# Optimization experiments

Hardware: AMD Instinct MI355X
Metric: run time of the kernel (lower is better)

Reference implementation:

```python
import jax, jax.numpy as jnp
import numpy as np
from jax import lax

TWN_THRESHOLD_FACTOR = 0.05
BN_EPS = 1e-5


@jax.custom_vjp
def _ternary_quant(w, t):
    return (w > t).astype(w.dtype) - (w < -t).astype(w.dtype)

def _tq_fwd(w, t):
    mask = (w > t) | (w < -t)
    return _ternary_quant(w, t), mask

def _tq_bwd(mask, g):
    return (g * mask.astype(g.dtype), jnp.zeros((), g.dtype))

_ternary_quant.defvjp(_tq_fwd, _tq_bwd)


def quantize(w):
    # threshold is detached in the original (weight.detach().abs().max())
    t = TWN_THRESHOLD_FACTOR * jnp.max(jnp.abs(lax.stop_gradient(w)))
    return _ternary_quant(w, t)


def conv2d(x, w, b):
    # x: [N,C,H,W], w: [O,I,K,K], valid conv, stride 1
    y = lax.conv_general_dilated(x, w, (1, 1), 'VALID',
                                 dimension_numbers=('NCHW', 'OIHW', 'NCHW'))
    return y + b[None, :, None, None]


def maxpool2(x):
    return lax.reduce_window(x, -jnp.inf, lax.max,
                             (1, 1, 2, 2), (1, 1, 2, 2), 'VALID')


def bn2d(x, g, b):
    # training-mode batch norm over (N,H,W), biased variance
    m = jnp.mean(x, (0, 2, 3), keepdims=True)
    v = jnp.mean(jnp.square(x - m), (0, 2, 3), keepdims=True)
    return (x - m) * lax.rsqrt(v + BN_EPS) * g[None, :, None, None] + b[None, :, None, None]


def bn1d(x, g, b):
    m = jnp.mean(x, 0, keepdims=True)
    v = jnp.mean(jnp.square(x - m), 0, keepdims=True)
    return (x - m) * lax.rsqrt(v + BN_EPS) * g[None, :] + b[None, :]


def setup_inputs() -> dict:
    key = jax.random.key(0)
    ks = jax.random.split(key, 12)
    N = 4096
    inp = {
        'x': jax.random.normal(ks[0], (N, 1, 28, 28), jnp.float32),
        'w1': jax.random.normal(ks[1], (32, 1, 5, 5), jnp.float32) * 0.2,
        'b1': jnp.zeros((32,), jnp.float32),
        'g1': jnp.ones((32,), jnp.float32),
        'be1': jnp.zeros((32,), jnp.float32),
        'w2': jax.random.normal(ks[2], (64, 32, 5, 5), jnp.float32) * 0.05,
        'b2': jnp.zeros((64,), jnp.float32),
        'g2': jnp.ones((64,), jnp.float32),
        'be2': jnp.zeros((64,), jnp.float32),
        'wf1': jax.random.normal(ks[3], (512, 1024), jnp.float32) * 0.03,
        'bf1': jnp.zeros((512,), jnp.float32),
        'g3': jnp.ones((512,), jnp.float32),
        'be3': jnp.zeros((512,), jnp.float32),
        'wf2': jax.random.normal(ks[4], (10, 512), jnp.float32) * 0.04,
        'bf2': jnp.zeros((10,), jnp.float32),
    }
    return inp


def reference(x, w1, b1, g1, be1, w2, b2, g2, be2, wf1, bf1, g3, be3, wf2, bf2):
    h = jax.nn.relu(bn2d(conv2d(x, quantize(w1), b1), g1, be1))     # [N,32,24,24]
    h = maxpool2(h)                                                  # [N,32,12,12]
    h = jax.nn.relu(bn2d(conv2d(h, quantize(w2), b2), g2, be2))     # [N,64,8,8]
    h = maxpool2(h)                                                  # [N,64,4,4]
    h = h.reshape(h.shape[0], -1)                                    # [N,1024]
    h = jax.nn.relu(bn1d(h @ quantize(wf1).T + bf1, g3, be3))       # [N,512]
    return h @ quantize(wf2).T + bf2                                 # [N,10]
```

## Files before the change

kernel.cpp:

```cpp
#include <hip/hip_runtime.h>

#define TID ((int)threadIdx.x)
typedef unsigned short u16;
typedef short short8 __attribute__((ext_vector_type(8)));
typedef float f32x4 __attribute__((ext_vector_type(4)));

__device__ __forceinline__ u16 f2b(float f) {
    unsigned int x = __float_as_uint(f);
    return (u16)((x + 0x7fffu + ((x >> 16) & 1u)) >> 16);
}
__device__ __forceinline__ float b2f(u16 u) {
    return __uint_as_float(((unsigned int)u) << 16);
}
__device__ __forceinline__ unsigned int cvt_pk(float lo, float hi) {
    unsigned int r;
    asm("v_cvt_pk_bf16_f32 %0, %1, %2" : "=v"(r) : "v"(lo), "v"(hi));
    return r;
}
__device__ __forceinline__ float xmax32(float w) {
    unsigned int a = __float_as_uint(w), b = a;
    asm("v_permlane32_swap_b32 %0, %1" : "+v"(a), "+v"(b));
    return fmaxf(__uint_as_float(a), __uint_as_float(b));
}

static constexpr size_t OFF_QW1   = 0;
static constexpr size_t OFF_QWF2  = 3200;
static constexpr size_t OFF_TMAX  = 23680;
static constexpr size_t OFF_SUM1C = 23808;
static constexpr size_t OFF_SSQ1C = 24832;
static constexpr size_t OFF_SUM2  = 25856, OFF_SSQ2 = 26112;
static constexpr size_t OFF_SUM3  = 26368, OFF_SSQ3 = 28416;
static constexpr size_t STATS_BEG = 23680, STATS_END = 30464;
static constexpr size_t OFF_QW2C  = 30720;
static constexpr size_t OFF_QWF1C = 133120;
static constexpr size_t OFF_Y1P   = 1181696;
static constexpr size_t OFF_H2P   = 38930432;
static constexpr size_t OFF_Y3    = 47319040;

__global__ __launch_bounds__(256) void absmax_k(const float* w1, const float* w2,
                                                const float* wf1, const float* wf2,
                                                unsigned int* tmaxbits) {
    int bid = blockIdx.x;
    int b, lb, nb; const float* src; long n;
    if (bid < 1)        { b = 0; src = w1;  n = 800;    lb = bid;       nb = 1;   }
    else if (bid < 9)   { b = 1; src = w2;  n = 51200;  lb = bid - 1;   nb = 8;   }
    else if (bid < 265) { b = 2; src = wf1; n = 524288; lb = bid - 9;   nb = 256; }
    else                { b = 3; src = wf2; n = 5120;   lb = bid - 265; nb = 1;   }
    float m = 0.f;
    for (long i = (long)lb * 256 + TID; i < n; i += (long)nb * 256)
        m = fmaxf(m, fabsf(src[i]));
    __shared__ float red[256];
    red[TID] = m; __syncthreads();
    for (int s = 128; s > 0; s >>= 1) {
        if (TID < s) red[TID] = fmaxf(red[TID], red[TID + s]);
        __syncthreads();
    }
    if (TID == 0) atomicMax(&tmaxbits[b], __float_as_uint(red[0]));
}

__global__ __launch_bounds__(256) void quant_all_k(const float* w1, const float* w2,
                                                   const float* wf1, const float* wf2,
                                                   float* qw1, u16* qw2c, u16* qwf1c,
                                                   float* qwf2, const unsigned int* tmax) {
    int bid = blockIdx.x;
    if (bid < 4) {
        int i = bid * 256 + TID; if (i >= 800) return;
        float t = 0.05f * __uint_as_float(tmax[0]);
        float v = w1[i];
        qw1[i] = (v > t) ? 1.f : ((v < -t) ? -1.f : 0.f);
    } else if (bid < 204) {
        int i = (bid - 4) * 256 + TID;
        float t = 0.05f * __uint_as_float(tmax[1]);
        int ic = i & 31, oc = (i >> 5) & 63, sh = i >> 11;
        float v = w2[(oc * 32 + ic) * 25 + sh];
        qw2c[i] = (v > t) ? (u16)0x3F80 : ((v < -t) ? (u16)0xBF80 : (u16)0);
    } else if (bid < 2252) {
        int i = (bid - 204) * 256 + TID;
        float t = 0.05f * __uint_as_float(tmax[2]);
        float v = wf1[i];
        qwf1c[i] = (v > t) ? (u16)0x3F80 : ((v < -t) ? (u16)0xBF80 : (u16)0);
    } else {
        int i = (bid - 2252) * 256 + TID;
        float t = 0.05f * __uint_as_float(tmax[3]);
        float v = wf2[i];
        qwf2[i] = (v > t) ? 1.f : ((v < -t) ? -1.f : 0.f);
    }
}

__global__ __launch_bounds__(256) void conv1_fused_k(const float* __restrict__ x,
                                                     const float* __restrict__ qw1,
                                                     u16* __restrict__ y1p,
                                                     float* sum1c, float* ssq1c) {
    __shared__ __align__(16) u16 xs[16 * 1096];
    int gid = blockIdx.x;
    int sg = gid >> 2, ph = (gid >> 1) & 1, pch = gid & 1;
    int l = TID & 63, w = TID >> 6;
    int lm = l & 15, q = l >> 4;

    #pragma unroll
    for (int i = 0; i < 9; i++) {
        int idx = TID + i * 256;
        if (idx < 2192) reinterpret_cast<uint4*>(xs)[idx] = make_uint4(0, 0, 0, 0);
    }

    short8 B1[2], B2[2];
    #pragma unroll
    for (int c = 0; c < 2; c++) {
        union { short8 s; u16 h[8]; } b1, b2;
        int ch = c * 16 + lm;
        #pragma unroll
        for (int j = 0; j < 8; j++) {
            float v1 = 0.f, v2 = 0.f;
            if (j < 5) {
                v1 = qw1[ch * 25 + q * 5 + j];
                v2 = qw1[ch * 25 + 20 + j];
            }
            b1.h[j] = f2b(v1);
            b2.h[j] = (q == 0) ? f2b(v2) : (u16)0;
        }
        B1[c] = b1.s; B2[c] = b2.s;
    }
    __syncthreads();

    #pragma unroll
    for (int k = 0; k < 7; k++) {
        int i = TID + k * 256;
        int smp = i / 112, rem = i % 112;
        int row = rem / 7, c4 = (rem % 7) * 4;
        float4 v = *reinterpret_cast<const float4*>(
            x + (size_t)(sg * 16 + smp) * 784 + (12 * ph + row) * 28 + c4);
        unsigned int r0 = cvt_pk(v.x, v.y), r1 = cvt_pk(v.z, v.w);
        uint2 pk; pk.x = r0; pk.y = r1;
        *reinterpret_cast<uint2*>(xs + smp * 1096 + row * 32 + c4) = pk;
        u16 h[4] = {(u16)r0, (u16)(r0 >> 16), (u16)r1, (u16)(r1 >> 16)};
        u16* b1p = xs + smp * 1096 + 548 + row * 32;
        #pragma unroll
        for (int e = 0; e < 4; e++) {
            int c = c4 + e;
            if (c >= 1) b1p[c - 1] = h[e];
        }
    }
    __syncthreads();

    float s0 = 0.f, s1 = 0.f, q0 = 0.f, q1 = 0.f;
    int laneoff = lm * 1096;
    #pragma unroll 1
    for (int e = 0; e < 9; e++) {
        int pp = w * 9 + e;
        int prl = pp / 6, pcl = pp - prl * 6;
        f32x4 pm0 = {-3.0e38f, -3.0e38f, -3.0e38f, -3.0e38f};
        f32x4 pm1 = pm0;
        #pragma unroll
        for (int dyx = 0; dyx < 4; dyx++) {
            int dy = dyx >> 1, dx = dyx & 1;
            int oyl = 2 * prl + dy;
            int ox = 2 * (pch * 6 + pcl) + dx;
            int r = ox & 1, cb = ox - r;
            const u16* p1 = xs + laneoff + r * 548 + (oyl + q) * 32 + cb;
            const u16* p2 = xs + laneoff + r * 548 + (oyl + 4) * 32 + cb;
            union { short8 s; unsigned int u[4]; } a1, a2;
            #pragma unroll
            for (int t = 0; t < 4; t++) {
                a1.u[t] = *reinterpret_cast<const unsigned int*>(p1 + 2 * t);
                a2.u[t] = *reinterpret_cast<const unsigned int*>(p2 + 2 * t);
            }
            f32x4 d0 = {0.f, 0.f, 0.f, 0.f};
            d0 = __builtin_amdgcn_mfma_f32_16x16x32_bf16(a1.s, B1[0], d0, 0, 0, 0);
            d0 = __builtin_amdgcn_mfma_f32_16x16x32_bf16(a2.s, B2[0], d0, 0, 0, 0);
            f32x4 d1 = {0.f, 0.f, 0.f, 0.f};
            d1 = __builtin_amdgcn_mfma_f32_16x16x32_bf16(a1.s, B1[1], d1, 0, 0, 0);
            d1 = __builtin_amdgcn_mfma_f32_16x16x32_bf16(a2.s, B2[1], d1, 0, 0, 0);
            #pragma unroll
            for (int i = 0; i < 4; i++) {
                float v = d0[i]; s0 += v; q0 = fmaf(v, v, q0);
                float u = d1[i]; s1 += u; q1 = fmaf(u, u, q1);
            }
            pm0 = __builtin_elementwise_max(pm0, d0);
            pm1 = __builtin_elementwise_max(pm1, d1);
        }
        int ppg = (ph * 6 + prl) * 12 + (pch * 6 + pcl);
        #pragma unroll
        for (int i = 0; i < 4; i++) {
            size_t nb = (size_t)(sg * 16 + 4 * q + i) * 4608 + ppg * 32;
            unsigned int r = cvt_pk(pm0[i], pm1[i]);
            y1p[nb + lm]      = (u16)r;
            y1p[nb + 16 + lm] = (u16)(r >> 16);
        }
    }
    s0 += __shfl_xor(s0, 16); s0 += __shfl_xor(s0, 32);
    s1 += __shfl_xor(s1, 16); s1 += __shfl_xor(s1, 32);
    q0 += __shfl_xor(q0, 16); q0 += __shfl_xor(q0, 32);
    q1 += __shfl_xor(q1, 16); q1 += __shfl_xor(q1, 32);
    if (l < 16) {
        int slot = (blockIdx.x & 7) * 32;
        atomicAdd(&sum1c[slot + l], s0);
        atomicAdd(&sum1c[slot + 16 + l], s1);
        atomicAdd(&ssq1c[slot + l], q0);
        atomicAdd(&ssq1c[slot + 16 + l], q1);
    }
}

__global__ __launch_bounds__(256) void conv2_k(const u16* __restrict__ y1p,
                                               const u16* __restrict__ qw2c,
                                               u16* __restrict__ h2pre,
                                               const float* sum1c, const float* ssq1c,
                                               const float* g1, const float* be1,
                                               float* sum, float* ssq) {
    __shared__ float4 hsm4[1176];
    __shared__ float scs[32], shs[32];
    char* hsraw = (char*)hsm4;
    int n0 = blockIdx.x * 8;
    int l = TID & 63, wv = TID >> 6;
    int oc0 = wv * 16;
    int lm = l & 15, lr = (l >> 3) & 1, ox = l & 7, bq = l >> 4;
    if (TID < 32) {
        float s = 0.f, q = 0.f;
        #pragma unroll
        for (int r = 0; r < 8; r++) { s += sum1c[r * 32 + TID]; q += ssq1c[r * 32 + TID]; }
        float m = s * (1.f / 2359296.f);
        float v = q * (1.f / 2359296.f) - m * m;
        float sc = g1[TID] / sqrtf(v + 1e-5f);
        scs[TID] = sc; shs[TID] = be1[TID] - m * sc;
    }
    __syncthreads();
    float scR[8], shR[8];
    {
        int b = TID & 3;
        #pragma unroll
        for (int j = 0; j < 8; j++) { scR[j] = scs[b * 8 + j]; shR[j] = shs[b * 8 + j]; }
    }
    short8 bw[25];
    #pragma unroll
    for (int sh = 0; sh < 25; sh++)
        bw[sh] = *reinterpret_cast<const short8*>(qw2c + ((size_t)sh * 64 + oc0 + lm) * 32 + bq * 8);
    int xy[5];
    #pragma unroll
    for (int kx = 0; kx < 5; kx++) {
        int xx = ox + kx;
        xy[kx] = lr * 784 + xx * 64 + (((bq + (xx >> 1)) & 3) * 16);
    }
    float sacc = 0.f, s2acc = 0.f;
    {
        const uint4* src = reinterpret_cast<const uint4*>(y1p + (size_t)n0 * 4608);
        #pragma unroll
        for (int k = 0; k < 3; k++) {
            if (k < 2 || TID < 64) {
                int i = TID + k * 256;
                int pix = i >> 2, b = i & 3;
                int y = pix / 12, xx = pix - y * 12;
                union { uint4 v; u16 u[8]; } in;
                in.v = src[i];
                float f[8];
                #pragma unroll
                for (int j = 0; j < 8; j++)
                    f[j] = fmaxf(fmaf(b2f(in.u[j]), scR[j], shR[j]), 0.f);
                uint4 o = make_uint4(cvt_pk(f[0], f[1]), cvt_pk(f[2], f[3]),
                                     cvt_pk(f[4], f[5]), cvt_pk(f[6], f[7]));
                *reinterpret_cast<uint4*>(hsraw + y * 784 + xx * 64 + (((b + (xx >> 1)) & 3) * 16)) = o;
            }
        }
    }
    #pragma unroll 1
    for (int s = 0; s < 8; s++) {
        __syncthreads();
        uint4 pf0 = {}, pf1 = {}, pf2 = {};
        if (s < 7) {
            const uint4* src = reinterpret_cast<const uint4*>(y1p + (size_t)(n0 + s + 1) * 4608);
            pf0 = src[TID];
            pf1 = src[TID + 256];
            if (TID < 64) pf2 = src[TID + 512];
        }
        const char* hb = hsraw + (s & 1) * 9408;
        f32x4 acc[4] = {{0.f,0.f,0.f,0.f},{0.f,0.f,0.f,0.f},{0.f,0.f,0.f,0.f},{0.f,0.f,0.f,0.f}};
        #pragma unroll
        for (int R = 0; R <= 10; R++) {
            short8 a[5];
            #pragma unroll
            for (int kx = 0; kx < 5; kx++)
                a[kx] = *reinterpret_cast<const short8*>(hb + xy[kx] + R * 784);
            #pragma unroll
            for (int mt = 0; mt < 4; mt++) {
                int ky = R - 2 * mt;
                if (ky < 0 || ky > 4) continue;
                #pragma unroll
                for (int kx = 0; kx < 5; kx++)
                    acc[mt] = __builtin_amdgcn_mfma_f32_16x16x32_bf16(a[kx], bw[ky * 5 + kx], acc[mt], 0, 0, 0);
            }
        }
        int n = n0 + s;
        u16* hp = h2pre + (size_t)n * 1024 + (oc0 + lm) * 16;
        #pragma unroll
        for (int mt = 0; mt < 4; mt++) {
            float v0 = acc[mt][0], v1 = acc[mt][1], v2 = acc[mt][2], v3 = acc[mt][3];
            sacc += v0 + v1 + v2 + v3;
            s2acc += v0 * v0 + v1 * v1 + v2 * v2 + v3 * v3;
            float w0 = fmaxf(v0, v1), w1 = fmaxf(v2, v3);
            float p0 = xmax32(w0);
            float p1 = xmax32(w1);
            if (bq < 2) {
                *reinterpret_cast<unsigned int*>(hp + mt * 4 + bq * 2) = cvt_pk(p0, p1);
            }
        }
        if (s < 7) {
            char* dst = hsraw + ((s + 1) & 1) * 9408;
            #pragma unroll
            for (int k = 0; k < 3; k++) {
                if (k < 2 || TID < 64) {
                    int i = TID + k * 256;
                    int pix = i >> 2, b = i & 3;
                    int y = pix / 12, xx = pix - y * 12;
                    union { uint4 v; u16 u[8]; } in;
                    in.v = (k == 0) ? pf0 : ((k == 1) ? pf1 : pf2);
                    float f[8];
                    #pragma unroll
                    for (int j = 0; j < 8; j++)
                        f[j] = fmaxf(fmaf(b2f(in.u[j]), scR[j], shR[j]), 0.f);
                    uint4 o = make_uint4(cvt_pk(f[0], f[1]), cvt_pk(f[2], f[3]),
                                         cvt_pk(f[4], f[5]), cvt_pk(f[6], f[7]));
                    *reinterpret_cast<uint4*>(dst + y * 784 + xx * 64 + (((b + (xx >> 1)) & 3) * 16)) = o;
                }
            }
        }
    }
    sacc  += __shfl_xor(sacc, 16);  sacc  += __shfl_xor(sacc, 32);
    s2acc += __shfl_xor(s2acc, 16); s2acc += __shfl_xor(s2acc, 32);
    if (l < 16) { atomicAdd(&sum[oc0 + l], sacc); atomicAdd(&ssq[oc0 + l], s2acc); }
}

__global__ __launch_bounds__(256) void fc1_k(const u16* __restrict__ h2pre,
                                             const u16* __restrict__ qwf1c,
                                             const float* sum2, const float* ssq2,
                                             const float* g2, const float* be2,
                                             float* __restrict__ y3T,
                                             float* sum3, float* ssq3) {
    __shared__ float4 Asm[2][576], Bsm[2][576];
    __shared__ float sc2s[64], sh2s[64];
    int m0 = blockIdx.x * 64, j0 = blockIdx.y * 64;
    int l = TID & 63, wv = TID >> 6;
    int lm = l & 15, q = l >> 4;
    int r0 = TID >> 3, c0 = TID & 7;
    if (TID < 64) {
        float m = sum2[TID] * (1.f / 262144.f);
        float v = ssq2[TID] * (1.f / 262144.f) - m * m;
        float s = g2[TID] / sqrtf(v + 1e-5f);
        sc2s[TID] = s; sh2s[TID] = be2[TID] - m * s;
    }
    __syncthreads();
    {
        u16* AsW = (u16*)Asm[0]; u16* BsW = (u16*)Bsm[0];
        int oc = (c0 * 8) >> 4;
        float sc = sc2s[oc], sh = sh2s[oc];
        #pragma unroll
        for (int i = 0; i < 2; i++) {
            int r = i * 32 + r0;
            union { float4 v; u16 h[8]; } in;
            in.v = *reinterpret_cast<const float4*>(h2pre + (size_t)(m0 + r) * 1024 + c0 * 8);
            float f[8];
            #pragma unroll
            for (int e = 0; e < 8; e++)
                f[e] = fmaxf(fmaf(b2f(in.h[e]), sc, sh), 0.f);
            uint4 o = make_uint4(cvt_pk(f[0], f[1]), cvt_pk(f[2], f[3]),
                                 cvt_pk(f[4], f[5]), cvt_pk(f[6], f[7]));
            *reinterpret_cast<uint4*>(AsW + r * 72 + c0 * 8) = o;
            *reinterpret_cast<float4*>(BsW + r * 72 + c0 * 8) =
                *reinterpret_cast<const float4*>(qwf1c + (size_t)(j0 + r) * 1024 + c0 * 8);
        }
    }
    f32x4 acc[4] = {{0.f,0.f,0.f,0.f},{0.f,0.f,0.f,0.f},{0.f,0.f,0.f,0.f},{0.f,0.f,0.f,0.f}};
    #pragma unroll 1
    for (int kc = 0; kc < 16; kc++) {
        __syncthreads();
        float4 pa0, pa1, pb0, pb1;
        if (kc < 15) {
            int kk = (kc + 1) * 64;
            pa0 = *reinterpret_cast<const float4*>(h2pre + (size_t)(m0 + r0) * 1024 + kk + c0 * 8);
            pa1 = *reinterpret_cast<const float4*>(h2pre + (size_t)(m0 + 32 + r0) * 1024 + kk + c0 * 8);
            pb0 = *reinterpret_cast<const float4*>(qwf1c + (size_t)(j0 + r0) * 1024 + kk + c0 * 8);
            pb1 = *reinterpret_cast<const float4*>(qwf1c + (size_t)(j0 + 32 + r0) * 1024 + kk + c0 * 8);
        }
        const u16* AsU = (const u16*)Asm[kc & 1];
        const u16* BsU = (const u16*)Bsm[kc & 1];
        #pragma unroll
        for (int half = 0; half < 2; half++) {
            short8 b = *reinterpret_cast<const short8*>(BsU + (wv * 16 + lm) * 72 + half * 32 + q * 8);
            #pragma unroll
            for (int mt = 0; mt < 4; mt++) {
                short8 a = *reinterpret_cast<const short8*>(AsU + (mt * 16 + lm) * 72 + half * 32 + q * 8);
                acc[mt] = __builtin_amdgcn_mfma_f32_16x16x32_bf16(a, b, acc[mt], 0, 0, 0);
            }
        }
        if (kc < 15) {
            int kk = (kc + 1) * 64;
            u16* AsW = (u16*)Asm[(kc + 1) & 1];
            u16* BsW = (u16*)Bsm[(kc + 1) & 1];
            int oc = (kk + c0 * 8) >> 4;
            float sc = sc2s[oc], sh = sh2s[oc];
            #pragma unroll
            for (int i = 0; i < 2; i++) {
                int r = i * 32 + r0;
                union { float4 v; u16 h[8]; } in;
                in.v = (i == 0) ? pa0 : pa1;
                float f[8];
                #pragma unroll
                for (int e = 0; e < 8; e++)
                    f[e] = fmaxf(fmaf(b2f(in.h[e]), sc, sh), 0.f);
                uint4 o = make_uint4(cvt_pk(f[0], f[1]), cvt_pk(f[2], f[3]),
                                     cvt_pk(f[4], f[5]), cvt_pk(f[6], f[7]));
                *reinterpret_cast<uint4*>(AsW + r * 72 + c0 * 8) = o;
                *reinterpret_cast<float4*>(BsW + r * 72 + c0 * 8) = (i == 0) ? pb0 : pb1;
            }
        }
    }
    float s = 0.f, s2 = 0.f;
    #pragma unroll
    for (int mt = 0; mt < 4; mt++) {
        *reinterpret_cast<f32x4*>(y3T + (size_t)(j0 + wv * 16 + lm) * 4096 + m0 + mt * 16 + q * 4) = acc[mt];
        #pragma unroll
        for (int i = 0; i < 4; i++) { float v = acc[mt][i]; s += v; s2 = fmaf(v, v, s2); }
    }
    s  += __shfl_xor(s, 16);  s  += __shfl_xor(s, 32);
    s2 += __shfl_xor(s2, 16); s2 += __shfl_xor(s2, 32);
    if (l < 16) {
        atomicAdd(&sum3[j0 + wv * 16 + l], s);
        atomicAdd(&ssq3[j0 + wv * 16 + l], s2);
    }
}

__global__ __launch_bounds__(256) void fc2_k(const float* __restrict__ y3T,
                                             const float* sum3, const float* ssq3,
                                             const float* g3, const float* be3,
                                             const float* __restrict__ qwf2,
                                             const float* bf2, float* __restrict__ out) {
    __shared__ float wlds[5120];
    __shared__ float part[15][160];
    __shared__ float sc3s[512], sh3s[512];
    for (int i = TID; i < 5120; i += 256) wlds[i] = qwf2[i];
    for (int k = TID; k < 512; k += 256) {
        float m = sum3[k] * (1.f / 4096.f);
        float v = ssq3[k] * (1.f / 4096.f) - m * m;
        float s = g3[k] / sqrtf(v + 1e-5f);
        sc3s[k] = s; sh3s[k] = be3[k] - m * s;
    }
    __syncthreads();
    int nl = TID & 15, ks = TID >> 4;
    int n = blockIdx.x * 16 + nl;
    float acc[10] = {};
    for (int k = ks * 32; k < ks * 32 + 32; k++) {
        float v = fmaxf(y3T[(size_t)k * 4096 + n] * sc3s[k] + sh3s[k], 0.f);
        #pragma unroll
        for (int o = 0; o < 10; o++) acc[o] = fmaf(v, wlds[o * 512 + k], acc[o]);
    }
    if (ks > 0) {
        #pragma unroll
        for (int o = 0; o < 10; o++) part[ks - 1][o * 16 + nl] = acc[o];
    }
    __syncthreads();
    if (ks == 0) {
        #pragma unroll
        for (int o = 0; o < 10; o++) {
            float r = acc[o] + bf2[o];
            #pragma unroll
            for (int j = 0; j < 15; j++) r += part[j][o * 16 + nl];
            out[n * 10 + o] = r;
        }
    }
}

extern "C" void kernel_launch(void* const* d_in, const int* in_sizes, int n_in,
                              void* d_out, int out_size, void* d_ws, size_t ws_size,
                              hipStream_t stream) {
    char* wsb = (char*)d_ws;
    const float* x   = (const float*)d_in[0];
    const float* w1  = (const float*)d_in[1];
    const float* g1  = (const float*)d_in[3];
    const float* be1 = (const float*)d_in[4];
    const float* w2  = (const float*)d_in[5];
    const float* g2  = (const float*)d_in[7];
    const float* be2 = (const float*)d_in[8];
    const float* wf1 = (const float*)d_in[9];
    const float* g3  = (const float*)d_in[11];
    const float* be3 = (const float*)d_in[12];
    const float* wf2 = (const float*)d_in[13];
    const float* bf2 = (const float*)d_in[14];
    float* out = (float*)d_out;

    unsigned int* tmax = (unsigned int*)(wsb + OFF_TMAX);
    float* qw1   = (float*)(wsb + OFF_QW1);
    float* qwf2  = (float*)(wsb + OFF_QWF2);
    u16*   qw2c  = (u16*)(wsb + OFF_QW2C);
    u16*   qwf1c = (u16*)(wsb + OFF_QWF1C);
    u16*   y1p   = (u16*)(wsb + OFF_Y1P);
    u16*   h2pre = (u16*)(wsb + OFF_H2P);
    float* y3    = (float*)(wsb + OFF_Y3);

    float* sum1c = (float*)(wsb + OFF_SUM1C); float* ssq1c = (float*)(wsb + OFF_SSQ1C);
    float* sum2  = (float*)(wsb + OFF_SUM2);  float* ssq2  = (float*)(wsb + OFF_SSQ2);
    float* sum3  = (float*)(wsb + OFF_SUM3);  float* ssq3  = (float*)(wsb + OFF_SSQ3);

    hipMemsetAsync(wsb + STATS_BEG, 0, STATS_END - STATS_BEG, stream);

    absmax_k<<<266, 256, 0, stream>>>(w1, w2, wf1, wf2, tmax);
    quant_all_k<<<2272, 256, 0, stream>>>(w1, w2, wf1, wf2, qw1, qw2c, qwf1c, qwf2, tmax);

    conv1_fused_k<<<1024, 256, 0, stream>>>(x, qw1, y1p, sum1c, ssq1c);
    conv2_k<<<512, 256, 0, stream>>>(y1p, qw2c, h2pre, sum1c, ssq1c, g1, be1, sum2, ssq2);
    fc1_k<<<dim3(64, 8), 256, 0, stream>>>(h2pre, qwf1c, sum2, ssq2, g2, be2, y3, sum3, ssq3);
    fc2_k<<<256, 256, 0, stream>>>(y3, sum3, ssq3, g3, be3, qwf2, bf2, out);
}
```

Baseline: 194.9 us.

## Process two samples per conv2 iteration, pooling in registers instead of permlane

Restructures conv2 so each wave's 16-row MFMA tile covers one output row from each of two samples, rather than two adjacent rows of one sample. Each loaded A fragment now feeds up to 25 MFMAs per iteration, and both vertical pool rows sit in the same lane, so the permlane32 swap is dropped. The shared buffer doubles to hold two samples per stage, the loop runs 4 iterations instead of 8, and there are twice the accumulators, which raises register pressure. A launch-bounds hint of 2 blocks per SIMD-group is added to cap that pressure.

```diff
diff --git a/kernel.cpp b/kernel.cpp
--- a/kernel.cpp
+++ b/kernel.cpp
@@ -16,11 +16,6 @@
     unsigned int r;
     asm("v_cvt_pk_bf16_f32 %0, %1, %2" : "=v"(r) : "v"(lo), "v"(hi));
     return r;
-}
-__device__ __forceinline__ float xmax32(float w) {
-    unsigned int a = __float_as_uint(w), b = a;
-    asm("v_permlane32_swap_b32 %0, %1" : "+v"(a), "+v"(b));
-    return fmaxf(__uint_as_float(a), __uint_as_float(b));
 }
 
 static constexpr size_t OFF_QW1   = 0;
@@ -200,19 +195,19 @@
     }
 }
 
-__global__ __launch_bounds__(256) void conv2_k(const u16* __restrict__ y1p,
-                                               const u16* __restrict__ qw2c,
-                                               u16* __restrict__ h2pre,
-                                               const float* sum1c, const float* ssq1c,
-                                               const float* g1, const float* be1,
-                                               float* sum, float* ssq) {
-    __shared__ float4 hsm4[1176];
+__global__ __launch_bounds__(256, 2) void conv2_k(const u16* __restrict__ y1p,
+                                                  const u16* __restrict__ qw2c,
+                                                  u16* __restrict__ h2pre,
+                                                  const float* sum1c, const float* ssq1c,
+                                                  const float* g1, const float* be1,
+                                                  float* sum, float* ssq) {
+    __shared__ float4 hsm4[2352];
     __shared__ float scs[32], shs[32];
     char* hsraw = (char*)hsm4;
     int n0 = blockIdx.x * 8;
     int l = TID & 63, wv = TID >> 6;
     int oc0 = wv * 16;
-    int lm = l & 15, lr = (l >> 3) & 1, ox = l & 7, bq = l >> 4;
+    int lm = l & 15, sp = (l >> 3) & 1, ox = l & 7, bq = l >> 4;
     if (TID < 32) {
         float s = 0.f, q = 0.f;
         #pragma unroll
@@ -237,87 +232,93 @@
     #pragma unroll
     for (int kx = 0; kx < 5; kx++) {
         int xx = ox + kx;
-        xy[kx] = lr * 784 + xx * 64 + (((bq + (xx >> 1)) & 3) * 16);
+        xy[kx] = sp * 9408 + xx * 64 + (((bq + (xx >> 1)) & 3) * 16);
     }
     float sacc = 0.f, s2acc = 0.f;
     {
         const uint4* src = reinterpret_cast<const uint4*>(y1p + (size_t)n0 * 4608);
         #pragma unroll
-        for (int k = 0; k < 3; k++) {
-            if (k < 2 || TID < 64) {
+        for (int k = 0; k < 5; k++) {
+            if (k < 4 || TID < 128) {
                 int i = TID + k * 256;
-                int pix = i >> 2, b = i & 3;
+                int smp = (i >= 576) ? 1 : 0;
+                int j = i - smp * 576;
+                int pix = j >> 2, b = j & 3;
                 int y = pix / 12, xx = pix - y * 12;
                 union { uint4 v; u16 u[8]; } in;
                 in.v = src[i];
                 float f[8];
                 #pragma unroll
-                for (int j = 0; j < 8; j++)
-                    f[j] = fmaxf(fmaf(b2f(in.u[j]), scR[j], shR[j]), 0.f);
+                for (int e = 0; e < 8; e++)
+                    f[e] = fmaxf(fmaf(b2f(in.u[e]), scR[e], shR[e]), 0.f);
                 uint4 o = make_uint4(cvt_pk(f[0], f[1]), cvt_pk(f[2], f[3]),
                                      cvt_pk(f[4], f[5]), cvt_pk(f[6], f[7]));
-                *reinterpret_cast<uint4*>(hsraw + y * 784 + xx * 64 + (((b + (xx >> 1)) & 3) * 16)) = o;
+                *reinterpret_cast<uint4*>(hsraw + smp * 9408 + y * 784 + xx * 64 +
+                                          (((b + (xx >> 1)) & 3) * 16)) = o;
             }
         }
     }
     #pragma unroll 1
-    for (int s = 0; s < 8; s++) {
+    for (int t = 0; t < 4; t++) {
         __syncthreads();
-        uint4 pf0 = {}, pf1 = {}, pf2 = {};
-        if (s < 7) {
-            const uint4* src = reinterpret_cast<const uint4*>(y1p + (size_t)(n0 + s + 1) * 4608);
-            pf0 = src[TID];
-            pf1 = src[TID + 256];
-            if (TID < 64) pf2 = src[TID + 512];
-        }
-        const char* hb = hsraw + (s & 1) * 9408;
-        f32x4 acc[4] = {{0.f,0.f,0.f,0.f},{0.f,0.f,0.f,0.f},{0.f,0.f,0.f,0.f},{0.f,0.f,0.f,0.f}};
-        #pragma unroll
-        for (int R = 0; R <= 10; R++) {
+        uint4 pf[5] = {};
+        if (t < 3) {
+            const uint4* src = reinterpret_cast<const uint4*>(y1p + (size_t)(n0 + 2 * (t + 1)) * 4608);
+            #pragma unroll
+            for (int k = 0; k < 5; k++)
+                if (k < 4 || TID < 128) pf[k] = src[TID + k * 256];
+        }
+        const char* hb = hsraw + (t & 1) * 18816;
+        f32x4 acc[8] = {{0.f,0.f,0.f,0.f},{0.f,0.f,0.f,0.f},{0.f,0.f,0.f,0.f},{0.f,0.f,0.f,0.f},
+                        {0.f,0.f,0.f,0.f},{0.f,0.f,0.f,0.f},{0.f,0.f,0.f,0.f},{0.f,0.f,0.f,0.f}};
+        #pragma unroll
+        for (int R = 0; R <= 11; R++) {
             short8 a[5];
             #pragma unroll
             for (int kx = 0; kx < 5; kx++)
                 a[kx] = *reinterpret_cast<const short8*>(hb + xy[kx] + R * 784);
             #pragma unroll
-            for (int mt = 0; mt < 4; mt++) {
-                int ky = R - 2 * mt;
+            for (int mt = 0; mt < 8; mt++) {
+                int ky = R - mt;
                 if (ky < 0 || ky > 4) continue;
                 #pragma unroll
                 for (int kx = 0; kx < 5; kx++)
                     acc[mt] = __builtin_amdgcn_mfma_f32_16x16x32_bf16(a[kx], bw[ky * 5 + kx], acc[mt], 0, 0, 0);
             }
         }
-        int n = n0 + s;
-        u16* hp = h2pre + (size_t)n * 1024 + (oc0 + lm) * 16;
-        #pragma unroll
-        for (int mt = 0; mt < 4; mt++) {
-            float v0 = acc[mt][0], v1 = acc[mt][1], v2 = acc[mt][2], v3 = acc[mt][3];
-            sacc += v0 + v1 + v2 + v3;
-            s2acc += v0 * v0 + v1 * v1 + v2 * v2 + v3 * v3;
-            float w0 = fmaxf(v0, v1), w1 = fmaxf(v2, v3);
-            float p0 = xmax32(w0);
-            float p1 = xmax32(w1);
-            if (bq < 2) {
-                *reinterpret_cast<unsigned int*>(hp + mt * 4 + bq * 2) = cvt_pk(p0, p1);
-            }
-        }
-        if (s < 7) {
-            char* dst = hsraw + ((s + 1) & 1) * 9408;
-            #pragma unroll
-            for (int k = 0; k < 3; k++) {
-                if (k < 2 || TID < 64) {
+        int n = n0 + 2 * t + (bq >> 1);
+        u16* hp = h2pre + (size_t)n * 1024 + (oc0 + lm) * 16 + (bq & 1) * 2;
+        #pragma unroll
+        for (int tp = 0; tp < 4; tp++) {
+            f32x4 A0 = acc[2 * tp], A1 = acc[2 * tp + 1];
+            float v0 = A0[0], v1 = A0[1], v2 = A0[2], v3 = A0[3];
+            float u0 = A1[0], u1 = A1[1], u2 = A1[2], u3 = A1[3];
+            sacc  += v0 + v1 + v2 + v3 + u0 + u1 + u2 + u3;
+            s2acc += v0*v0 + v1*v1 + v2*v2 + v3*v3 + u0*u0 + u1*u1 + u2*u2 + u3*u3;
+            float p0 = fmaxf(fmaxf(v0, v1), fmaxf(u0, u1));
+            float p1 = fmaxf(fmaxf(v2, v3), fmaxf(u2, u3));
+            *reinterpret_cast<unsigned int*>(hp + tp * 4) = cvt_pk(p0, p1);
+        }
+        if (t < 3) {
+            char* dst = hsraw + ((t + 1) & 1) * 18816;
+            #pragma unroll
+            for (int k = 0; k < 5; k++) {
+                if (k < 4 || TID < 128) {
                     int i = TID + k * 256;
-                    int pix = i >> 2, b = i & 3;
+                    int smp = (i >= 576) ? 1 : 0;
+                    int j = i - smp * 576;
+                    int pix = j >> 2, b = j & 3;
                     int y = pix / 12, xx = pix - y * 12;
                     union { uint4 v; u16 u[8]; } in;
-                    in.v = (k == 0) ? pf0 : ((k == 1) ? pf1 : pf2);
+                    in.v = pf[k];
                     float f[8];
                     #pragma unroll
-                    for (int j = 0; j < 8; j++)
-                        f[j] = fmaxf(fmaf(b2f(in.u[j]), scR[j], shR[j]), 0.f);
+                    for (int e = 0; e < 8; e++)
+                        f[e] = fmaxf(fmaf(b2f(in.u[e]), scR[e], shR[e]), 0.f);
                     uint4 o = make_uint4(cvt_pk(f[0], f[1]), cvt_pk(f[2], f[3]),
                                          cvt_pk(f[4], f[5]), cvt_pk(f[6], f[7]));
-                    *reinterpret_cast<uint4*>(dst + y * 784 + xx * 64 + (((b + (xx >> 1)) & 3) * 16)) = o;
+                    *reinterpret_cast<uint4*>(dst + smp * 9408 + y * 784 + xx * 64 +
+                                              (((b + (xx >> 1)) & 3) * 16)) = o;
                 }
             }
         }
```

Result: faster. 189.0 us, median of 3 (-3.0%).
